# Optimization experiments

Hardware: AMD Instinct MI355X
Metric: run time of the kernel (lower is better)

The kernel has to match this reference:

```python
import jax, jax.numpy as jnp
import numpy as np

N_TASK, N_RET, N_DRAM, N_LINK = 50000, 20000, 5000, 100000
E_RET, E_DRAM, E_LINK = 1_000_000, 250_000, 2_000_000
H = 64


def setup_inputs() -> dict:
    key = jax.random.key(0)
    k = jax.random.split(key, 17)
    s = 1.0 / np.sqrt(3 * H)
    return {
        "feat_ret":  jax.random.normal(k[0], (E_RET, 1), jnp.float32),
        "feat_dram": jax.random.normal(k[1], (E_DRAM, 1), jnp.float32),
        "feat_link": jax.random.normal(k[2], (E_LINK, 1), jnp.float32),
        "W_ret":  jax.random.normal(k[3], (H, 1), jnp.float32),
        "b_ret":  jax.random.normal(k[4], (H,), jnp.float32) * 0.1,
        "W_dram": jax.random.normal(k[5], (H, 1), jnp.float32),
        "b_dram": jax.random.normal(k[6], (H,), jnp.float32) * 0.1,
        "W_link": jax.random.normal(k[7], (H, 1), jnp.float32),
        "b_link": jax.random.normal(k[8], (H,), jnp.float32) * 0.1,
        "W_task": jax.random.normal(k[9], (H, 3 * H), jnp.float32) * s,
        "b_task": jax.random.normal(k[10], (H,), jnp.float32) * 0.1,
        "task_ret":  jax.random.randint(k[11], (E_RET,), 0, N_TASK),
        "mod_ret":   jax.random.randint(k[12], (E_RET,), 0, N_RET),
        "task_dram": jax.random.randint(k[13], (E_DRAM,), 0, N_TASK),
        "mod_dram":  jax.random.randint(k[14], (E_DRAM,), 0, N_DRAM),
        "task_link": jax.random.randint(k[15], (E_LINK,), 0, N_TASK),
        "mod_link":  jax.random.randint(k[16], (E_LINK,), 0, N_LINK),
    }


def _gather_inp(feat, mod_idx, n_mod, W, b):
    # use_X: copy_e('feat') + sum per module node, then Linear(1,H) + tanh (activate_inp)
    inp = jax.ops.segment_sum(feat, mod_idx, num_segments=n_mod)  # [n_mod, 1]
    return jnp.tanh(inp @ W.T + b)                                # [n_mod, H]


def _max_to_task(inp_mod, mod_idx, task_idx, n_task):
    # X_used_by: copy_u('inp') + max per task node; zero-in-degree tasks -> 0 (DGL convention)
    m = jax.ops.segment_max(inp_mod[mod_idx], task_idx, num_segments=n_task)
    deg = jax.ops.segment_sum(jnp.ones_like(task_idx), task_idx, num_segments=n_task)
    return jnp.where((deg > 0)[:, None], m, 0.0)


def reference(feat_ret, feat_dram, feat_link, W_ret, b_ret, W_dram, b_dram,
              W_link, b_link, W_task, b_task,
              task_ret, mod_ret, task_dram, mod_dram, task_link, mod_link):
    # _module_update_inp
    inp_ret  = _gather_inp(feat_ret,  mod_ret,  N_RET,  W_ret,  b_ret)
    inp_dram = _gather_inp(feat_dram, mod_dram, N_DRAM, W_dram, b_dram)
    inp_link = _gather_inp(feat_link, mod_link, N_LINK, W_link, b_link)

    # _task_update_h: per-etype max reduce, cross-etype concat, Linear(3H,H) + tanh
    h_cat = jnp.concatenate([
        _max_to_task(inp_ret,  mod_ret,  task_ret,  N_TASK),
        _max_to_task(inp_dram, mod_dram, task_dram, N_TASK),
        _max_to_task(inp_link, mod_link, task_link, N_TASK),
    ], axis=-1)                                                   # [N_TASK, 3H]
    h_task = jnp.tanh(h_cat @ W_task.T + b_task)                  # [N_TASK, H]

    # _module_update_h: use_link copy_u('h') + mean per link node
    s = jax.ops.segment_sum(h_task[task_link], mod_link, num_segments=N_LINK)
    deg = jax.ops.segment_sum(jnp.ones((E_LINK,), jnp.float32), mod_link, num_segments=N_LINK)
    h_link = jnp.where((deg > 0)[:, None], s / jnp.maximum(deg, 1.0)[:, None], 0.0)
    return h_link
```

## Files before the change

kernel.cpp:

```cpp
#include <hip/hip_runtime.h>
#include <stdint.h>

#define N_TASK 50000
#define N_RET 20000
#define N_DRAM 5000
#define N_LINK 100000
#define E_RET 1000000
#define E_DRAM 250000
#define E_LINK 2000000

#define SBE 4096
#define NS_RET 245
#define NS_DRAM 62
#define NS_LINK 489
#define NS_TOT (NS_RET + NS_DRAM + NS_LINK)
#define MR_RET 64
#define RSZ_RET 313
#define MR_DRAM 16
#define RSZ_DRAM 313
#define MR_LINK 256
#define RSZ_LINK 391
#define RECIP313 107203u
#define RECIP391 85817u
#define CAPM_RET 16250
#define CAPM_DRAM 16250
#define CAPM_LINK 8255
#define BM4_RET 0
#define BM4_DRAM (MR_RET * NS_RET)
#define BM4_LINK (BM4_DRAM + MR_DRAM * NS_DRAM)
#define BM4_TOT (BM4_LINK + MR_LINK * NS_LINK)
#define BT_RET 0
#define BT_DRAM (16 * NS_RET)
#define BT_LINK (BT_DRAM + 16 * NS_DRAM)
#define BT_TOT (BT_LINK + 16 * NS_LINK)

#define R_PART 3125
#define CAP_RET 63800
#define CAP_DRAM 16300
#define CAP_LINK 126800
#define SUB_RET 4
#define SUB_DRAM 1
#define SUB_LINK 8
#define PB_RET 0
#define PB_DRAM (16 * SUB_RET * R_PART)
#define PB_LINK (PB_DRAM + 16 * SUB_DRAM * R_PART)
#define PB_TOT (PB_LINK + 16 * SUB_LINK * R_PART)

#define WS_SRET 0
#define WS_SDRAM 80000
#define WS_SLINK 100000
#define WS_CNT 500000
#define WS_OFFS 900000
#define WS_TMAX 1300000
#define WS_TMIN 1900000
#define WS_BCNT 2500000
#define WS_RCNT 2500192
#define WS_CSR 2501536
#define WS_BLKM 10501536
#define WS_BLKB 11068960
#define WS_MREC_RET 15701536
#define WS_MREC_DRAM 24021536
#define WS_MREC_LINK 26101536
#define WS_PART1 15701536
#define WS_HPL0_1 20901536
#define WS_HPL1_1 24101536
#define WS_TREC32_RET 43007776
#define WS_TREC32_DRAM 47090976
#define WS_TREC32_LINK 48134176
#define WS_WTB_1 56249376
#define WS_NEED1 56273952
#define WS_PART2 10501536
#define WS_TREC_RET 15701536
#define WS_TREC_DRAM 23867936
#define WS_TREC_LINK 25954336
#define WS_HPL0_2 15701536
#define WS_HPL1_2 18901536
#define WS_WTB_2 43007776
#define WS_NEED2 43032352

typedef __attribute__((ext_vector_type(8))) short bf16x8;
typedef __attribute__((ext_vector_type(4))) float f32x4;
typedef unsigned long long u64;

__device__ __forceinline__ unsigned ford(float f) {
  unsigned u = __float_as_uint(f);
  return (u & 0x80000000u) ? ~u : (u | 0x80000000u);
}
__device__ __forceinline__ float funord(unsigned t) {
  unsigned u = (t & 0x80000000u) ? (t & 0x7fffffffu) : ~t;
  return __uint_as_float(u);
}
__device__ __forceinline__ unsigned short bf16rne(float f) {
  unsigned u = __float_as_uint(f);
  return (unsigned short)((u + 0x7fffu + ((u >> 16) & 1u)) >> 16);
}

__device__ __forceinline__ void decode_sblk(int bx, int& e, int& blk, int& E0, int& NB,
                                            int& NR, unsigned& RECIP, int& RSZ, int& base) {
  if (bx < NS_RET) {
    e = 0; blk = bx; E0 = E_RET; NB = NS_RET; NR = MR_RET; RECIP = RECIP313; RSZ = RSZ_RET; base = BM4_RET;
  } else if (bx < NS_RET + NS_DRAM) {
    e = 1; blk = bx - NS_RET; E0 = E_DRAM; NB = NS_DRAM; NR = MR_DRAM; RECIP = RECIP313; RSZ = RSZ_DRAM; base = BM4_DRAM;
  } else {
    e = 2; blk = bx - NS_RET - NS_DRAM; E0 = E_LINK; NB = NS_LINK; NR = MR_LINK; RECIP = RECIP391; RSZ = RSZ_LINK; base = BM4_LINK;
  }
}
__device__ __forceinline__ void decode_stblk(int bx, int& e, int& blk, int& E0, int& NB,
                                             int& baset) {
  if (bx < NS_RET) { e = 0; blk = bx; E0 = E_RET; NB = NS_RET; baset = BT_RET; }
  else if (bx < NS_RET + NS_DRAM) { e = 1; blk = bx - NS_RET; E0 = E_DRAM; NB = NS_DRAM; baset = BT_DRAM; }
  else { e = 2; blk = bx - NS_RET - NS_DRAM; E0 = E_LINK; NB = NS_LINK; baset = BT_LINK; }
}


__global__ __launch_bounds__(256) void k_count3(
    const int* __restrict__ mr, const int* __restrict__ md, const int* __restrict__ ml,
    const float* __restrict__ W_task, unsigned short* __restrict__ wtb,
    int* __restrict__ blkcnt_m, int* __restrict__ tcur) {
  int bx = blockIdx.x, tid = threadIdx.x;
  if (bx == NS_TOT + 48) {
    if (tid < 48) tcur[tid] = 0;
    return;
  }
  if (bx >= NS_TOT) {
    int i = (bx - NS_TOT) * 256 + tid;
    if (i < 64 * 192) wtb[i] = bf16rne(W_task[i]);
    return;
  }
  __shared__ int c[256];
  int e, blk, E0, NB, NR, RSZ, base; unsigned RECIP;
  decode_sblk(bx, e, blk, E0, NB, NR, RECIP, RSZ, base);
  const int* mod = (e == 0) ? mr : (e == 1) ? md : ml;
  c[tid] = 0;
  __syncthreads();
  int i0 = blk * SBE;
#pragma unroll
  for (int q = 0; q < 16; q++) {
    int i = i0 + q * 256 + tid;
    if (i < E0) {
      int m = mod[i];
      int r = (int)(((u64)(unsigned)m * RECIP) >> 25);
      atomicAdd(&c[r], 1);
    }
  }
  __syncthreads();
  for (int r = tid; r < NR; r += 256)
    blkcnt_m[base + r * NB + blk] = c[r];
}

__global__ __launch_bounds__(512) void k_scan3(const int* __restrict__ blkcnt_m,
                                               int* __restrict__ blkbase_m,
                                               int* __restrict__ rcnt) {
  __shared__ int sm[512];
  int gb = blockIdx.x, tid = threadIdx.x;
  int NB, off;
  if (gb < 64) { NB = NS_RET; off = BM4_RET + gb * NS_RET; }
  else if (gb < 80) { NB = NS_DRAM; off = BM4_DRAM + (gb - 64) * NS_DRAM; }
  else { NB = NS_LINK; off = BM4_LINK + (gb - 80) * NS_LINK; }
  int v = (tid < NB) ? blkcnt_m[off + tid] : 0;
  sm[tid] = v;
  __syncthreads();
  for (int d = 1; d < 512; d <<= 1) {
    int x = (tid >= d) ? sm[tid - d] : 0;
    __syncthreads();
    sm[tid] += x;
    __syncthreads();
  }
  if (tid < NB) blkbase_m[off + tid] = sm[tid] - v;
  if (tid == 511) rcnt[gb] = sm[511];
}

__global__ __launch_bounds__(512) void k_mscatter3(
    const int* __restrict__ mr, const int* __restrict__ md, const int* __restrict__ ml,
    const int* __restrict__ tr, const int* __restrict__ td, const int* __restrict__ tl,
    const float* __restrict__ fr, const float* __restrict__ fd, const float* __restrict__ fl,
    const int* __restrict__ blkcnt_m, const int* __restrict__ blkbase_m,
    u64* __restrict__ mrec_ret, u64* __restrict__ mrec_dram, u64* __restrict__ mrec_link) {
  __shared__ int lcur[256];
  __shared__ int pdelta[256];
  __shared__ int sscan[256];
  __shared__ u64 srec[SBE];
  __shared__ int sdelta[SBE];
  int tid = threadIdx.x;
  int e, blk, E0, NB, NR, RSZ, base; unsigned RECIP;
  decode_sblk(blockIdx.x, e, blk, E0, NB, NR, RECIP, RSZ, base);
  const int* mod = (e == 0) ? mr : (e == 1) ? md : ml;
  const int* task = (e == 0) ? tr : (e == 1) ? td : tl;
  const float* feat = (e == 0) ? fr : (e == 1) ? fd : fl;
  u64* out = (e == 0) ? mrec_ret : (e == 1) ? mrec_dram : mrec_link;
  int CAP = (e == 0) ? CAPM_RET : (e == 1) ? CAPM_DRAM : CAPM_LINK;
  int cnt_r = 0, base_r = 0;
  if (tid < NR) {
    cnt_r = blkcnt_m[base + tid * NB + blk];
    base_r = blkbase_m[base + tid * NB + blk];
  }
  if (tid < 256) sscan[tid] = cnt_r;
  __syncthreads();
  for (int d = 1; d < 256; d <<= 1) {
    int x = (tid < 256 && tid >= d) ? sscan[tid - d] : 0;
    __syncthreads();
    if (tid < 256) sscan[tid] += x;
    __syncthreads();
  }
  if (tid < 256) {
    int excl = sscan[tid] - cnt_r;
    lcur[tid] = excl;
    pdelta[tid] = tid * CAP + base_r - excl;
  }
  __syncthreads();
  int i0 = blk * SBE;
#pragma unroll
  for (int q = 0; q < 8; q++) {
    int i = i0 + q * 512 + tid;
    if (i < E0) {
      int m = mod[i];
      int r = (int)(((u64)(unsigned)m * RECIP) >> 25);
      unsigned mloc = (unsigned)(m - r * RSZ);
      unsigned tk = (unsigned)task[i];
      unsigned fu = __float_as_uint(feat[i]);
      int slot = atomicAdd(&lcur[r], 1);
      srec[slot] = ((u64)fu << 32) | (tk << 16) | mloc;
      int gpos = pdelta[r] + slot - r * CAP;
      sdelta[slot] = (gpos < CAP) ? pdelta[r] : (int)0x80000000;
    }
  }
  __syncthreads();
  int total = E0 - i0; if (total > SBE) total = SBE;
  for (int s = tid; s < total; s += 512) {
    int d = sdelta[s];
    if (d != (int)0x80000000) out[d + s] = srec[s];
  }
}

#define P1BODY(rec, moff) { \
  int mloc_ = (int)((rec) & 0xFFFFull) + (moff); \
  int task_ = (int)(((rec) >> 16) & 0xFFFFull); \
  atomicAdd(&ssum[mloc_], __uint_as_float((unsigned)((rec) >> 32))); \
  if (e == 2) atomicAdd(&scnt[mloc_], 1); \
  atomicAdd(&tcnt16[w][task_ / R_PART], 1); }

#define P3BODY(rec, moff) { \
  int mloc_ = (int)((rec) & 0xFFFFull) + (moff); \
  int task_ = (int)(((rec) >> 16) & 0xFFFFull); \
  if (e == 2) { int lp_ = atomicAdd(&soff[mloc_], 1); csr[rb + lp_] = task_; } \
  int b_ = task_ / R_PART; \
  unsigned tl12_ = (unsigned)(task_ - b_ * R_PART); \
  unsigned u_ = (ford(ssum[mloc_]) & 0xFFFFF000u) | tl12_; \
  int local_ = atomicAdd(&tcnt16[w][b_], 1); \
  int pos_ = tbase16[w][b_] + local_; \
  if (pos_ < CAPT) trec[(long)b_ * CAPT + pos_] = u_; }

__global__ __launch_bounds__(1024) void k_msum3(
    const u64* __restrict__ mrec_ret, const u64* __restrict__ mrec_dram,
    const u64* __restrict__ mrec_link, const int* __restrict__ rcnt,
    int* __restrict__ cnt, int* __restrict__ offs, int* __restrict__ csr,
    int* __restrict__ tcur,
    unsigned* __restrict__ trec_ret, unsigned* __restrict__ trec_dram,
    unsigned* __restrict__ trec_link) {
  __shared__ float ssum[2 * RSZ_LINK];
  __shared__ int scnt[2 * RSZ_LINK];
  __shared__ int soff[2 * RSZ_LINK + 1];
  __shared__ int red[1024];
  __shared__ int tcnt16[16][16];
  __shared__ int tbase16[16][16];
  int gb = blockIdx.x, tid = threadIdx.x;
  int w = tid >> 6;
  int e, m0, nmod, RSZtot, CAPT, rl0 = 0;
  int cnt0, cnt1 = 0;
  const u64 *p0, *p1 = nullptr;
  unsigned* trec;
  if (gb < MR_RET) {
    e = 0; p0 = mrec_ret + (long)gb * CAPM_RET;
    cnt0 = rcnt[gb]; if (cnt0 > CAPM_RET) cnt0 = CAPM_RET;
    RSZtot = RSZ_RET; m0 = gb * RSZ_RET; nmod = N_RET - m0;
    CAPT = CAP_RET; trec = trec_ret;
  } else if (gb < MR_RET + MR_DRAM) {
    e = 1; int rl = gb - MR_RET; p0 = mrec_dram + (long)rl * CAPM_DRAM;
    cnt0 = rcnt[gb]; if (cnt0 > CAPM_DRAM) cnt0 = CAPM_DRAM;
    RSZtot = RSZ_DRAM; m0 = rl * RSZ_DRAM; nmod = N_DRAM - m0;
    CAPT = CAP_DRAM; trec = trec_dram;
  } else {
    e = 2; rl0 = 2 * (gb - (MR_RET + MR_DRAM));
    p0 = mrec_link + (long)rl0 * CAPM_LINK; p1 = p0 + CAPM_LINK;
    cnt0 = rcnt[80 + rl0]; if (cnt0 > CAPM_LINK) cnt0 = CAPM_LINK;
    cnt1 = rcnt[80 + rl0 + 1]; if (cnt1 > CAPM_LINK) cnt1 = CAPM_LINK;
    RSZtot = 2 * RSZ_LINK; m0 = rl0 * RSZ_LINK; nmod = N_LINK - m0;
    CAPT = CAP_LINK; trec = trec_link;
  }
  if (nmod > RSZtot) nmod = RSZtot;
  for (int j = tid; j < RSZtot; j += 1024) { ssum[j] = 0.f; scnt[j] = 0; }
  if (tid < 256) tcnt16[tid >> 4][tid & 15] = 0;
  __syncthreads();
  {
    int i = tid;
    for (; i + 3072 < cnt0; i += 4096) {
      u64 a = p0[i], b = p0[i + 1024], c = p0[i + 2048], d = p0[i + 3072];
      P1BODY(a, 0) P1BODY(b, 0) P1BODY(c, 0) P1BODY(d, 0)
    }
    for (; i < cnt0; i += 1024) { u64 a = p0[i]; P1BODY(a, 0) }
    if (e == 2) {
      i = tid;
      for (; i + 3072 < cnt1; i += 4096) {
        u64 a = p1[i], b = p1[i + 1024], c = p1[i + 2048], d = p1[i + 3072];
        P1BODY(a, RSZ_LINK) P1BODY(b, RSZ_LINK) P1BODY(c, RSZ_LINK) P1BODY(d, RSZ_LINK)
      }
      for (; i < cnt1; i += 1024) { u64 a = p1[i]; P1BODY(a, RSZ_LINK) }
    }
  }
  __syncthreads();
  if (tid < 16) {
    int b2 = tid, tot = 0;
    for (int w2 = 0; w2 < 16; w2++) { tbase16[w2][b2] = tot; tot += tcnt16[w2][b2]; }
    int g0 = atomicAdd(&tcur[e * 16 + b2], tot);
    for (int w2 = 0; w2 < 16; w2++) { tbase16[w2][b2] += g0; tcnt16[w2][b2] = 0; }
  }
  int rb = 0;
  if (e == 2) {
    int partial = (tid < 256 && tid < rl0) ? rcnt[80 + tid] : 0;
    if (tid < 256) red[tid] = partial;
    __syncthreads();
    for (int s = 128; s > 0; s >>= 1) {
      if (tid < s) red[tid] += red[tid + s];
      __syncthreads();
    }
    rb = red[0];
    __syncthreads();
    int vv = (tid < nmod) ? scnt[tid] : 0;
    red[tid] = vv;
    __syncthreads();
    for (int d = 1; d < 1024; d <<= 1) {
      int x = (tid >= d) ? red[tid - d] : 0;
      __syncthreads();
      red[tid] += x;
      __syncthreads();
    }
    if (tid < nmod) soff[tid] = red[tid] - vv;
    __syncthreads();
    for (int j = tid; j < nmod; j += 1024) {
      cnt[m0 + j] = scnt[j];
      offs[m0 + j] = rb + soff[j];
    }
  }
  __syncthreads();
  {
    int i = tid;
    for (; i + 3072 < cnt0; i += 4096) {
      u64 a = p0[i], b = p0[i + 1024], c = p0[i + 2048], d = p0[i + 3072];
      P3BODY(a, 0) P3BODY(b, 0) P3BODY(c, 0) P3BODY(d, 0)
    }
    for (; i < cnt0; i += 1024) { u64 a = p0[i]; P3BODY(a, 0) }
    if (e == 2) {
      i = tid;
      for (; i + 3072 < cnt1; i += 4096) {
        u64 a = p1[i], b = p1[i + 1024], c = p1[i + 2048], d = p1[i + 3072];
        P3BODY(a, RSZ_LINK) P3BODY(b, RSZ_LINK) P3BODY(c, RSZ_LINK) P3BODY(d, RSZ_LINK)
      }
      for (; i < cnt1; i += 1024) { u64 a = p1[i]; P3BODY(a, RSZ_LINK) }
    }
  }
}
#undef P1BODY
#undef P3BODY

#define PBBODY(rec) { \
  unsigned r_ = (rec) & 0xFFFu; \
  atomicMax(&lmax[r_], (rec)); \
  atomicMin(&lmin[r_], (rec)); }

__global__ __launch_bounds__(1024) void k_passb3(
    const unsigned* __restrict__ trec_ret, const unsigned* __restrict__ trec_dram,
    const unsigned* __restrict__ trec_link,
    const int* __restrict__ tcur, unsigned* __restrict__ partials) {
  __shared__ unsigned lmax[R_PART];
  __shared__ unsigned lmin[R_PART];
  int blk = blockIdx.x, tid = threadIdx.x;
  int e, b, sub, Nb, PB, CAP;
  const unsigned* bkt;
  if (blk < 16 * SUB_RET) {
    e = 0; b = blk >> 2; sub = blk & 3; Nb = SUB_RET; PB = PB_RET; CAP = CAP_RET; bkt = trec_ret;
  } else if (blk < 16 * (SUB_RET + SUB_DRAM)) {
    int q = blk - 16 * SUB_RET;
    e = 1; b = q; sub = 0; Nb = SUB_DRAM; PB = PB_DRAM; CAP = CAP_DRAM; bkt = trec_dram;
  } else {
    int q = blk - 16 * (SUB_RET + SUB_DRAM);
    e = 2; b = q >> 3; sub = q & 7; Nb = SUB_LINK; PB = PB_LINK; CAP = CAP_LINK; bkt = trec_link;
  }
  for (int idx = tid; idx < R_PART; idx += 1024) {
    lmax[idx] = 0u;
    lmin[idx] = 0xFFFFFFFFu;
  }
  __syncthreads();
  int count = tcur[e * 16 + b];
  if (count > CAP) count = CAP;
  int chunk = (count + Nb - 1) / Nb;
  int s0 = sub * chunk;
  int s1 = s0 + chunk; if (s1 > count) s1 = count;
  const unsigned* p = bkt + (long)b * CAP;
  int i = s0 + tid;
  for (; i + 3072 < s1; i += 4096) {
    unsigned r0 = p[i], r1 = p[i + 1024], r2 = p[i + 2048], r3 = p[i + 3072];
    PBBODY(r0) PBBODY(r1) PBBODY(r2) PBBODY(r3)
  }
  for (; i < s1; i += 1024) { unsigned r0 = p[i]; PBBODY(r0) }
  __syncthreads();
  unsigned gbase = PB + (unsigned)(b * Nb + sub) * R_PART;
  for (int idx = tid; idx < R_PART; idx += 1024) {
    partials[gbase + idx] = lmax[idx];
    partials[PB_TOT + gbase + idx] = lmin[idx];
  }
}
#undef PBBODY

__global__ __launch_bounds__(256) void k_mmred3(const unsigned* __restrict__ partials,
                                                unsigned* __restrict__ tmax,
                                                unsigned* __restrict__ tmin) {
  int gid = blockIdx.x * 256 + threadIdx.x;
  if (gid >= 3 * N_TASK) return;
  int e = gid / N_TASK;
  int t = gid - e * N_TASK;
  int Nb = (e == 0) ? SUB_RET : (e == 1) ? SUB_DRAM : SUB_LINK;
  int PB = (e == 0) ? PB_RET : (e == 1) ? PB_DRAM : PB_LINK;
  int b = t / R_PART;
  int r = t - b * R_PART;
  unsigned umax = 0u, umin = 0xFFFFFFFFu;
  for (int sub = 0; sub < Nb; sub++) {
    unsigned idx = PB + (unsigned)(b * Nb + sub) * R_PART + r;
    unsigned wv = partials[idx];
    if (wv > umax) umax = wv;
    unsigned w2 = partials[PB_TOT + idx];
    if (w2 < umin) umin = w2;
  }
  tmax[gid] = umax & 0xFFFFF000u;
  tmin[gid] = umin & 0xFFFFF000u;
}


__global__ __launch_bounds__(256) void k_count(
    const int* __restrict__ mr, const int* __restrict__ md, const int* __restrict__ ml,
    const int* __restrict__ tr, const int* __restrict__ td, const int* __restrict__ tl,
    const float* __restrict__ W_task, unsigned short* __restrict__ wtb,
    int* __restrict__ blkcnt_m, int* __restrict__ blkcnt_t) {
  int bx = blockIdx.x, tid = threadIdx.x;
  if (bx >= 2 * NS_TOT) {
    int i = (bx - 2 * NS_TOT) * 256 + tid;
    if (i < 64 * 192) wtb[i] = bf16rne(W_task[i]);
    return;
  }
  __shared__ int c[256];
  c[tid] = 0;
  __syncthreads();
  if (bx < NS_TOT) {
    int e, blk, E0, NB, NR, RSZ, base; unsigned RECIP;
    decode_sblk(bx, e, blk, E0, NB, NR, RECIP, RSZ, base);
    const int* mod = (e == 0) ? mr : (e == 1) ? md : ml;
    int i0 = blk * SBE;
#pragma unroll
    for (int q = 0; q < 16; q++) {
      int i = i0 + q * 256 + tid;
      if (i < E0) {
        int m = mod[i];
        int r = (int)(((u64)(unsigned)m * RECIP) >> 25);
        atomicAdd(&c[r], 1);
      }
    }
    __syncthreads();
    for (int r = tid; r < NR; r += 256)
      blkcnt_m[base + r * NB + blk] = c[r];
  } else {
    int e, blk, E0, NB, baset;
    decode_stblk(bx - NS_TOT, e, blk, E0, NB, baset);
    const int* task = (e == 0) ? tr : (e == 1) ? td : tl;
    int i0 = blk * SBE;
#pragma unroll
    for (int q = 0; q < 16; q++) {
      int i = i0 + q * 256 + tid;
      if (i < E0) atomicAdd(&c[task[i] / R_PART], 1);
    }
    __syncthreads();
    if (tid < 16) blkcnt_t[baset + tid * NB + blk] = c[tid];
  }
}

__global__ __launch_bounds__(512) void k_scan(int* __restrict__ blkcnt_m,
                                              int* __restrict__ blkcnt_t,
                                              int* __restrict__ rcnt, int* __restrict__ bcnt) {
  __shared__ int sm[512];
  int gb = blockIdx.x, tid = threadIdx.x;
  int* arr; int NB; int* outp;
  if (gb < 336) {
    int off;
    if (gb < 64) { NB = NS_RET; off = BM4_RET + gb * NS_RET; }
    else if (gb < 80) { NB = NS_DRAM; off = BM4_DRAM + (gb - 64) * NS_DRAM; }
    else { NB = NS_LINK; off = BM4_LINK + (gb - 80) * NS_LINK; }
    arr = blkcnt_m + off; outp = rcnt + gb;
  } else {
    int g = gb - 336; int e = g >> 4, b = g & 15;
    int NBe = (e == 0) ? NS_RET : (e == 1) ? NS_DRAM : NS_LINK;
    int baset = (e == 0) ? BT_RET : (e == 1) ? BT_DRAM : BT_LINK;
    NB = NBe; arr = blkcnt_t + baset + b * NBe; outp = bcnt + g;
  }
  int v = (tid < NB) ? arr[tid] : 0;
  sm[tid] = v;
  __syncthreads();
  for (int d = 1; d < 512; d <<= 1) {
    int x = (tid >= d) ? sm[tid - d] : 0;
    __syncthreads();
    sm[tid] += x;
    __syncthreads();
  }
  if (tid < NB) arr[tid] = sm[tid] - v;
  if (tid == 511) *outp = sm[511];
}

__global__ __launch_bounds__(256) void k_mscatter2(
    const int* __restrict__ mr, const int* __restrict__ md, const int* __restrict__ ml,
    const int* __restrict__ tl,
    const float* __restrict__ fr, const float* __restrict__ fd, const float* __restrict__ fl,
    const int* __restrict__ blkcnt_m,
    u64* __restrict__ mrec_ret, u64* __restrict__ mrec_dram, u64* __restrict__ mrec_link) {
  __shared__ int lcur[256];
  __shared__ int pdelta[256];
  __shared__ int sscan[256];
  __shared__ u64 srec[SBE];
  __shared__ int sdelta[SBE];
  int tid = threadIdx.x;
  int e, blk, E0, NB, NR, RSZ, base; unsigned RECIP;
  decode_sblk(blockIdx.x, e, blk, E0, NB, NR, RECIP, RSZ, base);
  const int* mod = (e == 0) ? mr : (e == 1) ? md : ml;
  const float* feat = (e == 0) ? fr : (e == 1) ? fd : fl;
  u64* out = (e == 0) ? mrec_ret : (e == 1) ? mrec_dram : mrec_link;
  int CAP = (e == 0) ? CAPM_RET : (e == 1) ? CAPM_DRAM : CAPM_LINK;
  lcur[tid] = 0;
  __syncthreads();
  int i0 = blk * SBE;
#pragma unroll
  for (int q = 0; q < 16; q++) {
    int i = i0 + q * 256 + tid;
    if (i < E0) {
      int m = mod[i];
      int r = (int)(((u64)(unsigned)m * RECIP) >> 25);
      atomicAdd(&lcur[r], 1);
    }
  }
  __syncthreads();
  int v = lcur[tid];
  sscan[tid] = v;
  __syncthreads();
  for (int d = 1; d < 256; d <<= 1) {
    int x = (tid >= d) ? sscan[tid - d] : 0;
    __syncthreads();
    sscan[tid] += x;
    __syncthreads();
  }
  int excl = sscan[tid] - v;
  int total = sscan[255];
  int gbv = (tid < NR) ? blkcnt_m[base + tid * NB + blk] : 0;
  __syncthreads();
  lcur[tid] = excl;
  pdelta[tid] = tid * CAP + gbv - excl;
  __syncthreads();
#pragma unroll
  for (int q = 0; q < 16; q++) {
    int i = i0 + q * 256 + tid;
    if (i < E0) {
      int m = mod[i];
      int r = (int)(((u64)(unsigned)m * RECIP) >> 25);
      unsigned mloc = (unsigned)(m - r * RSZ);
      unsigned task = (e == 2) ? (unsigned)tl[i] : 0u;
      unsigned fu = __float_as_uint(feat[i]);
      int slot = atomicAdd(&lcur[r], 1);
      srec[slot] = ((u64)fu << 32) | (task << 16) | mloc;
      int gpos = pdelta[r] + slot - r * CAP;
      sdelta[slot] = (gpos < CAP) ? pdelta[r] : (int)0x80000000;
    }
  }
  __syncthreads();
  for (int s = tid; s < total; s += 256) {
    int d = sdelta[s];
    if (d != (int)0x80000000) out[d + s] = srec[s];
  }
}

__global__ __launch_bounds__(256) void k_msum(
    const u64* __restrict__ mrec_ret, const u64* __restrict__ mrec_dram,
    const u64* __restrict__ mrec_link, const int* __restrict__ rcnt,
    float* __restrict__ s_ret, float* __restrict__ s_dram, float* __restrict__ s_link,
    int* __restrict__ cnt, int* __restrict__ offs, int* __restrict__ csr) {
  __shared__ float ssum[RSZ_LINK];
  __shared__ int scnt[RSZ_LINK];
  __shared__ int soff[RSZ_LINK + 1];
  __shared__ int red[256];
  int gb = blockIdx.x, tid = threadIdx.x;
  int e, rl, RSZ, CAP, Ntot;
  const u64* p;
  float* sout;
  if (gb < MR_RET) {
    e = 0; rl = gb; p = mrec_ret + (long)rl * CAPM_RET; sout = s_ret;
    RSZ = RSZ_RET; CAP = CAPM_RET; Ntot = N_RET;
  } else if (gb < MR_RET + MR_DRAM) {
    e = 1; rl = gb - MR_RET; p = mrec_dram + (long)rl * CAPM_DRAM; sout = s_dram;
    RSZ = RSZ_DRAM; CAP = CAPM_DRAM; Ntot = N_DRAM;
  } else {
    e = 2; rl = gb - MR_RET - MR_DRAM; p = mrec_link + (long)rl * CAPM_LINK; sout = s_link;
    RSZ = RSZ_LINK; CAP = CAPM_LINK; Ntot = N_LINK;
  }
  int m0 = rl * RSZ;
  int nmod = Ntot - m0; if (nmod > RSZ) nmod = RSZ;
  for (int j = tid; j < RSZ; j += 256) { ssum[j] = 0.f; scnt[j] = 0; }
  __syncthreads();
  int count = rcnt[gb]; if (count > CAP) count = CAP;
  for (int i = tid; i < count; i += 256) {
    u64 rec = p[i];
    int mloc = (int)(rec & 0xFFFFull);
    atomicAdd(&ssum[mloc], __uint_as_float((unsigned)(rec >> 32)));
    if (e == 2) atomicAdd(&scnt[mloc], 1);
  }
  __syncthreads();
  for (int j = tid; j < nmod; j += 256) sout[m0 + j] = ssum[j];
  if (e != 2) return;
  int partial = (80 + tid < gb) ? rcnt[80 + tid] : 0;
  red[tid] = partial;
  __syncthreads();
  for (int s = 128; s > 0; s >>= 1) {
    if (tid < s) red[tid] += red[tid + s];
    __syncthreads();
  }
  int rb = red[0];
  __syncthreads();
  int a0 = (2 * tid < nmod) ? scnt[2 * tid] : 0;
  int a1 = (2 * tid + 1 < nmod) ? scnt[2 * tid + 1] : 0;
  red[tid] = a0 + a1;
  __syncthreads();
  for (int d = 1; d < 256; d <<= 1) {
    int x = (tid >= d) ? red[tid - d] : 0;
    __syncthreads();
    red[tid] += x;
    __syncthreads();
  }
  int excl = red[tid] - (a0 + a1);
  if (2 * tid < RSZ_LINK) soff[2 * tid] = excl;
  if (2 * tid + 1 < RSZ_LINK) soff[2 * tid + 1] = excl + a0;
  __syncthreads();
  for (int j = tid; j < nmod; j += 256) {
    cnt[m0 + j] = scnt[j];
    offs[m0 + j] = rb + soff[j];
  }
  __syncthreads();
  for (int i = tid; i < count; i += 256) {
    u64 rec = p[i];
    int mloc = (int)(rec & 0xFFFFull);
    int task = (int)((rec >> 16) & 0xFFFFull);
    int lp = atomicAdd(&soff[mloc], 1);
    csr[rb + lp] = task;
  }
}

__global__ __launch_bounds__(256) void k_ascatter2(
    const int* __restrict__ tr, const int* __restrict__ mr,
    const int* __restrict__ td, const int* __restrict__ md,
    const int* __restrict__ tl, const int* __restrict__ ml,
    const float* __restrict__ s_ret, const float* __restrict__ s_dram,
    const float* __restrict__ s_link, const int* __restrict__ blkcnt_t,
    u64* __restrict__ trec_ret, u64* __restrict__ trec_dram, u64* __restrict__ trec_link) {
  __shared__ int lcur[256];
  __shared__ int pdelta[256];
  __shared__ int sscan[256];
  __shared__ u64 srec[SBE];
  __shared__ int sdelta[SBE];
  int tid = threadIdx.x;
  int e, blk, E0, NB, baset;
  decode_stblk(blockIdx.x, e, blk, E0, NB, baset);
  const int* task = (e == 0) ? tr : (e == 1) ? td : tl;
  const int* mod = (e == 0) ? mr : (e == 1) ? md : ml;
  const float* s = (e == 0) ? s_ret : (e == 1) ? s_dram : s_link;
  u64* out = (e == 0) ? trec_ret : (e == 1) ? trec_dram : trec_link;
  int CAP = (e == 0) ? CAP_RET : (e == 1) ? CAP_DRAM : CAP_LINK;
  lcur[tid] = 0;
  __syncthreads();
  int i0 = blk * SBE;
#pragma unroll
  for (int q = 0; q < 16; q++) {
    int i = i0 + q * 256 + tid;
    if (i < E0) atomicAdd(&lcur[task[i] / R_PART], 1);
  }
  __syncthreads();
  int v = lcur[tid];
  sscan[tid] = v;
  __syncthreads();
  for (int d = 1; d < 256; d <<= 1) {
    int x = (tid >= d) ? sscan[tid - d] : 0;
    __syncthreads();
    sscan[tid] += x;
    __syncthreads();
  }
  int excl = sscan[tid] - v;
  int total = sscan[255];
  int gbv = (tid < 16) ? blkcnt_t[baset + tid * NB + blk] : 0;
  __syncthreads();
  lcur[tid] = excl;
  pdelta[tid] = tid * CAP + gbv - excl;
  __syncthreads();
#pragma unroll
  for (int q = 0; q < 16; q++) {
    int i = i0 + q * 256 + tid;
    if (i < E0) {
      int t = task[i];
      int r = t / R_PART;
      unsigned rloc = (unsigned)(t - r * R_PART);
      unsigned u = ford(s[mod[i]]);
      int slot = atomicAdd(&lcur[r], 1);
      srec[slot] = ((u64)u << 32) | rloc;
      int gpos = pdelta[r] + slot - r * CAP;
      sdelta[slot] = (gpos < CAP) ? pdelta[r] : (int)0x80000000;
    }
  }
  __syncthreads();
  for (int sidx = tid; sidx < total; sidx += 256) {
    int d = sdelta[sidx];
    if (d != (int)0x80000000) out[d + sidx] = srec[sidx];
  }
}

__global__ __launch_bounds__(256) void k_passb(
    const u64* __restrict__ trec_ret, const u64* __restrict__ trec_dram,
    const u64* __restrict__ trec_link,
    const int* __restrict__ bcnt, unsigned* __restrict__ partials) {
  __shared__ unsigned lmax[R_PART];
  __shared__ unsigned lmin[R_PART];
  int blk = blockIdx.x;
  int e, b, sub, Nb, PB, CAP;
  const u64* bkt;
  if (blk < 16 * SUB_RET) {
    e = 0; b = blk >> 2; sub = blk & 3; Nb = SUB_RET; PB = PB_RET; CAP = CAP_RET; bkt = trec_ret;
  } else if (blk < 16 * (SUB_RET + SUB_DRAM)) {
    int q = blk - 16 * SUB_RET;
    e = 1; b = q; sub = 0; Nb = SUB_DRAM; PB = PB_DRAM; CAP = CAP_DRAM; bkt = trec_dram;
  } else {
    int q = blk - 16 * (SUB_RET + SUB_DRAM);
    e = 2; b = q >> 3; sub = q & 7; Nb = SUB_LINK; PB = PB_LINK; CAP = CAP_LINK; bkt = trec_link;
  }
  for (int idx = threadIdx.x; idx < R_PART; idx += 256) {
    lmax[idx] = 0u;
    lmin[idx] = 0xFFFFFFFFu;
  }
  __syncthreads();
  int count = bcnt[e * 16 + b];
  if (count > CAP) count = CAP;
  int chunk = (count + Nb - 1) / Nb;
  int s0 = sub * chunk;
  int s1 = s0 + chunk; if (s1 > count) s1 = count;
  const u64* p = bkt + (long)b * CAP;
  for (int i = s0 + threadIdx.x; i < s1; i += 256) {
    u64 rec = p[i];
    unsigned r = (unsigned)rec;
    unsigned u = (unsigned)(rec >> 32);
    atomicMax(&lmax[r], u);
    atomicMin(&lmin[r], u);
  }
  __syncthreads();
  unsigned gbase = PB + (unsigned)(b * Nb + sub) * R_PART;
  for (int idx = threadIdx.x; idx < R_PART; idx += 256) {
    partials[gbase + idx] = lmax[idx];
    partials[PB_TOT + gbase + idx] = lmin[idx];
  }
}

__global__ __launch_bounds__(256) void k_mmred2(const unsigned* __restrict__ partials,
                                                unsigned* __restrict__ tmax,
                                                unsigned* __restrict__ tmin) {
  int gid = blockIdx.x * 256 + threadIdx.x;
  if (gid >= 3 * N_TASK) return;
  int e = gid / N_TASK;
  int t = gid - e * N_TASK;
  int Nb = (e == 0) ? SUB_RET : (e == 1) ? SUB_DRAM : SUB_LINK;
  int PB = (e == 0) ? PB_RET : (e == 1) ? PB_DRAM : PB_LINK;
  int b = t / R_PART;
  int r = t - b * R_PART;
  unsigned umax = 0u, umin = 0xFFFFFFFFu;
  for (int sub = 0; sub < Nb; sub++) {
    unsigned idx = PB + (unsigned)(b * Nb + sub) * R_PART + r;
    unsigned wv = partials[idx];
    if (wv > umax) umax = wv;
    unsigned w2 = partials[PB_TOT + idx];
    if (w2 < umin) umin = w2;
  }
  tmax[gid] = umax;
  tmin[gid] = umin;
}


__global__ void k_wprep(const float* __restrict__ W_task, unsigned short* __restrict__ wtb) {
  int i = blockIdx.x * 256 + threadIdx.x;
  if (i < 64 * 192) wtb[i] = bf16rne(W_task[i]);
}

__global__ void f_segsum(const float* __restrict__ fr, const float* __restrict__ fd,
                         const float* __restrict__ fl,
                         const int* __restrict__ mr, const int* __restrict__ md,
                         const int* __restrict__ ml,
                         float* s_ret, float* s_dram, float* s_link, int* cnt) {
  int i = blockIdx.x * blockDim.x + threadIdx.x;
  const int total = E_RET + E_DRAM + E_LINK;
  if (i >= total) return;
  if (i < E_RET) {
    atomicAdd(&s_ret[mr[i]], fr[i]);
  } else if (i < E_RET + E_DRAM) {
    int j = i - E_RET;
    atomicAdd(&s_dram[md[j]], fd[j]);
  } else {
    int j = i - (E_RET + E_DRAM);
    int m = ml[j];
    atomicAdd(&s_link[m], fl[j]);
    atomicAdd(&cnt[m], 1);
  }
}

__global__ void f_minmax(const float* __restrict__ s_ret, const float* __restrict__ s_dram,
                         const float* __restrict__ s_link,
                         const int* __restrict__ tr, const int* __restrict__ mr,
                         const int* __restrict__ td, const int* __restrict__ md,
                         const int* __restrict__ tl, const int* __restrict__ ml,
                         unsigned* tmax, unsigned* tmin) {
  int i = blockIdx.x * blockDim.x + threadIdx.x;
  const int total = E_RET + E_DRAM + E_LINK;
  if (i >= total) return;
  int e, task; unsigned u;
  if (i < E_RET) {
    u = ford(s_ret[mr[i]]); task = tr[i]; e = 0;
  } else if (i < E_RET + E_DRAM) {
    int j = i - E_RET;
    u = ford(s_dram[md[j]]); task = td[j]; e = 1;
  } else {
    int j = i - (E_RET + E_DRAM);
    u = ford(s_link[ml[j]]); task = tl[j]; e = 2;
  }
  atomicMax(&tmax[e * N_TASK + task], u);
  atomicMin(&tmin[e * N_TASK + task], u);
}

__global__ void f_part(const int* __restrict__ cnt, int* part) {
  __shared__ int sm[256];
  int i = blockIdx.x * 256 + threadIdx.x;
  sm[threadIdx.x] = (i < N_LINK) ? cnt[i] : 0;
  __syncthreads();
  for (int s = 128; s > 0; s >>= 1) {
    if (threadIdx.x < s) sm[threadIdx.x] += sm[threadIdx.x + s];
    __syncthreads();
  }
  if (threadIdx.x == 0) part[blockIdx.x] = sm[0];
}

__global__ void f_scanpart(const int* __restrict__ part, int* partx, int npart) {
  __shared__ int sm[512];
  int t = threadIdx.x;
  int v = (t < npart) ? part[t] : 0;
  sm[t] = v;
  __syncthreads();
  for (int d = 1; d < 512; d <<= 1) {
    int x = (t >= d) ? sm[t - d] : 0;
    __syncthreads();
    sm[t] += x;
    __syncthreads();
  }
  if (t < npart) partx[t] = sm[t] - v;
}

__global__ void f_offs(const int* __restrict__ cnt, const int* __restrict__ partx,
                       int* offs, int* cursor) {
  __shared__ int sm[256];
  int i = blockIdx.x * 256 + threadIdx.x;
  int t = threadIdx.x;
  int v = (i < N_LINK) ? cnt[i] : 0;
  sm[t] = v;
  __syncthreads();
  for (int d = 1; d < 256; d <<= 1) {
    int x = (t >= d) ? sm[t - d] : 0;
    __syncthreads();
    sm[t] += x;
    __syncthreads();
  }
  if (i < N_LINK) {
    int o = partx[blockIdx.x] + sm[t] - v;
    offs[i] = o;
    cursor[i] = o;
  }
}

__global__ void f_scatter(const int* __restrict__ tl, const int* __restrict__ ml,
                          int* cursor, int* csr) {
  int i = blockIdx.x * blockDim.x + threadIdx.x;
  if (i >= E_LINK) return;
  int pos = atomicAdd(&cursor[ml[i]], 1);
  csr[pos] = tl[i];
}


__global__ __launch_bounds__(256) void k_taskm(
    const float* __restrict__ W_ret, const float* __restrict__ b_ret,
    const float* __restrict__ W_dram, const float* __restrict__ b_dram,
    const float* __restrict__ W_link, const float* __restrict__ b_link,
    const unsigned short* __restrict__ wtb, const float* __restrict__ b_task,
    const unsigned* __restrict__ tmax, const unsigned* __restrict__ tmin,
    unsigned short* __restrict__ hp0, unsigned short* __restrict__ hp1) {
  int wave = threadIdx.x >> 6;
  int lane = threadIdx.x & 63;
  int tile = blockIdx.x * 4 + wave;
  if (tile >= N_TASK / 16) return;
  int t0 = tile * 16;
  int l16 = lane & 15;
  int quad = lane >> 4;
  int t = t0 + l16;

  f32x4 acc[4];
#pragma unroll
  for (int nf = 0; nf < 4; nf++) acc[nf] = (f32x4){0.f, 0.f, 0.f, 0.f};

  const float* We[3] = {W_ret, W_dram, W_link};
  const float* be[3] = {b_ret, b_dram, b_link};

  for (int e = 0; e < 3; e++) {
    unsigned um = tmax[e * N_TASK + t];
    float smax = funord(um);
    float smin = funord(tmin[e * N_TASK + t]);
    bool live = (um != 0u);
#pragma unroll
    for (int h = 0; h < 2; h++) {
      int kb = h * 32 + quad * 8;
      float4 w0 = *(const float4*)&We[e][kb];
      float4 w1 = *(const float4*)&We[e][kb + 4];
      float4 b0 = *(const float4*)&be[e][kb];
      float4 b1 = *(const float4*)&be[e][kb + 4];
      float wv[8] = {w0.x, w0.y, w0.z, w0.w, w1.x, w1.y, w1.z, w1.w};
      float bv[8] = {b0.x, b0.y, b0.z, b0.w, b1.x, b1.y, b1.z, b1.w};
      bf16x8 afrag;
#pragma unroll
      for (int j = 0; j < 8; j++) {
        float wj = wv[j];
        float ss = (wj >= 0.f) ? smax : smin;
        float hc = live ? tanhf(fmaf(ss, wj, bv[j])) : 0.f;
        afrag[j] = (short)bf16rne(hc);
      }
      int kk = e * 64 + h * 32 + quad * 8;
#pragma unroll
      for (int nf = 0; nf < 4; nf++) {
        int o = nf * 16 + l16;
        bf16x8 bfrag = *(const bf16x8*)&wtb[o * 192 + kk];
        acc[nf] = __builtin_amdgcn_mfma_f32_16x16x32_bf16(afrag, bfrag, acc[nf], 0, 0, 0);
      }
    }
  }

#pragma unroll
  for (int nf = 0; nf < 4; nf++) {
    int n = nf * 16 + l16;
    float bt = b_task[n];
    unsigned short* hp = (n < 32) ? hp0 : hp1;
    int f = n & 31;
#pragma unroll
    for (int r = 0; r < 4; r++) {
      int m = quad * 4 + r;
      float v = tanhf(acc[nf][r] + bt);
      hp[(t0 + m) * 32 + f] = bf16rne(v);
    }
  }
}

__global__ __launch_bounds__(256) void k_link2(const unsigned short* __restrict__ hp,
                                               const int* __restrict__ offs,
                                               const int* __restrict__ cnt,
                                               const int* __restrict__ csr,
                                               float* __restrict__ out, int plane) {
  int l = blockIdx.x * 8 + (threadIdx.x >> 5);
  int f = threadIdx.x & 31;
  int start = offs[l];
  int c = cnt[l];
  float acc = 0.f;
  for (int q = 0; q < c; q += 4) {
    int i1 = (q + 1 < c) ? q + 1 : c - 1;
    int i2 = (q + 2 < c) ? q + 2 : c - 1;
    int i3 = (q + 3 < c) ? q + 3 : c - 1;
    int t0 = csr[start + q];
    int t1 = csr[start + i1];
    int t2 = csr[start + i2];
    int t3 = csr[start + i3];
    unsigned v0 = hp[t0 * 32 + f];
    unsigned v1 = hp[t1 * 32 + f];
    unsigned v2 = hp[t2 * 32 + f];
    unsigned v3 = hp[t3 * 32 + f];
    acc += __uint_as_float(v0 << 16);
    if (q + 1 < c) acc += __uint_as_float(v1 << 16);
    if (q + 2 < c) acc += __uint_as_float(v2 << 16);
    if (q + 3 < c) acc += __uint_as_float(v3 << 16);
  }
  out[l * 64 + plane * 32 + f] = (c > 0) ? acc / (float)c : 0.f;
}

extern "C" void kernel_launch(void* const* d_in, const int* in_sizes, int n_in,
                              void* d_out, int out_size, void* d_ws, size_t ws_size,
                              hipStream_t stream) {
  const float* feat_ret  = (const float*)d_in[0];
  const float* feat_dram = (const float*)d_in[1];
  const float* feat_link = (const float*)d_in[2];
  const float* W_ret  = (const float*)d_in[3];
  const float* b_ret  = (const float*)d_in[4];
  const float* W_dram = (const float*)d_in[5];
  const float* b_dram = (const float*)d_in[6];
  const float* W_link = (const float*)d_in[7];
  const float* b_link = (const float*)d_in[8];
  const float* W_task = (const float*)d_in[9];
  const float* b_task = (const float*)d_in[10];
  const int* task_ret  = (const int*)d_in[11];
  const int* mod_ret   = (const int*)d_in[12];
  const int* task_dram = (const int*)d_in[13];
  const int* mod_dram  = (const int*)d_in[14];
  const int* task_link = (const int*)d_in[15];
  const int* mod_link  = (const int*)d_in[16];
  float* out = (float*)d_out;

  char* ws = (char*)d_ws;
  float* s_ret  = (float*)(ws + WS_SRET);
  float* s_dram = (float*)(ws + WS_SDRAM);
  float* s_link = (float*)(ws + WS_SLINK);
  int*   cnt    = (int*)(ws + WS_CNT);
  int*   offs   = (int*)(ws + WS_OFFS);
  unsigned* tmax = (unsigned*)(ws + WS_TMAX);
  unsigned* tmin = (unsigned*)(ws + WS_TMIN);
  int* tcur = (int*)(ws + WS_BCNT);
  int* rcnt = (int*)(ws + WS_RCNT);
  int* csr  = (int*)(ws + WS_CSR);
  int* blkcnt_m = (int*)(ws + WS_BLKM);
  int* blkb = (int*)(ws + WS_BLKB);
  u64* mrec_ret  = (u64*)(ws + WS_MREC_RET);
  u64* mrec_dram = (u64*)(ws + WS_MREC_DRAM);
  u64* mrec_link = (u64*)(ws + WS_MREC_LINK);

  unsigned short* hp0;
  unsigned short* hp1;
  unsigned short* wtb;

  if (ws_size >= (size_t)WS_NEED1) {
    unsigned* partials = (unsigned*)(ws + WS_PART1);
    unsigned* trec_ret  = (unsigned*)(ws + WS_TREC32_RET);
    unsigned* trec_dram = (unsigned*)(ws + WS_TREC32_DRAM);
    unsigned* trec_link = (unsigned*)(ws + WS_TREC32_LINK);
    hp0 = (unsigned short*)(ws + WS_HPL0_1);
    hp1 = (unsigned short*)(ws + WS_HPL1_1);
    wtb = (unsigned short*)(ws + WS_WTB_1);
    k_count3<<<NS_TOT + 49, 256, 0, stream>>>(mod_ret, mod_dram, mod_link,
                                              W_task, wtb, blkcnt_m, tcur);
    k_scan3<<<336, 512, 0, stream>>>(blkcnt_m, blkb, rcnt);
    k_mscatter3<<<NS_TOT, 512, 0, stream>>>(mod_ret, mod_dram, mod_link,
                                            task_ret, task_dram, task_link,
                                            feat_ret, feat_dram, feat_link,
                                            blkcnt_m, blkb,
                                            mrec_ret, mrec_dram, mrec_link);
    k_msum3<<<MR_RET + MR_DRAM + MR_LINK / 2, 1024, 0, stream>>>(
        mrec_ret, mrec_dram, mrec_link, rcnt,
        cnt, offs, csr, tcur,
        trec_ret, trec_dram, trec_link);
    k_passb3<<<16 * (SUB_RET + SUB_DRAM + SUB_LINK), 1024, 0, stream>>>(
        trec_ret, trec_dram, trec_link, tcur, partials);
    k_mmred3<<<(3 * N_TASK + 255) / 256, 256, 0, stream>>>(partials, tmax, tmin);
  } else if (ws_size >= (size_t)WS_NEED2) {
    unsigned* partials = (unsigned*)(ws + WS_PART2);
    u64* trec_ret  = (u64*)(ws + WS_TREC_RET);
    u64* trec_dram = (u64*)(ws + WS_TREC_DRAM);
    u64* trec_link = (u64*)(ws + WS_TREC_LINK);
    hp0 = (unsigned short*)(ws + WS_HPL0_2);
    hp1 = (unsigned short*)(ws + WS_HPL1_2);
    wtb = (unsigned short*)(ws + WS_WTB_2);
    k_count<<<2 * NS_TOT + 48, 256, 0, stream>>>(mod_ret, mod_dram, mod_link,
                                                 task_ret, task_dram, task_link,
                                                 W_task, wtb, blkcnt_m, blkb);
    k_scan<<<384, 512, 0, stream>>>(blkcnt_m, blkb, rcnt, tcur);
    k_mscatter2<<<NS_TOT, 256, 0, stream>>>(mod_ret, mod_dram, mod_link, task_link,
                                            feat_ret, feat_dram, feat_link, blkcnt_m,
                                            mrec_ret, mrec_dram, mrec_link);
    k_msum<<<336, 256, 0, stream>>>(mrec_ret, mrec_dram, mrec_link, rcnt,
                                    s_ret, s_dram, s_link, cnt, offs, csr);
    k_ascatter2<<<NS_TOT, 256, 0, stream>>>(task_ret, mod_ret, task_dram, mod_dram,
                                            task_link, mod_link, s_ret, s_dram, s_link,
                                            blkb, trec_ret, trec_dram, trec_link);
    k_passb<<<16 * (SUB_RET + SUB_DRAM + SUB_LINK), 256, 0, stream>>>(
        trec_ret, trec_dram, trec_link, tcur, partials);
    k_mmred2<<<(3 * N_TASK + 255) / 256, 256, 0, stream>>>(partials, tmax, tmin);
  } else {
    int* part   = (int*)(ws + WS_BLKM);
    int* partx  = (int*)(ws + WS_BLKM + 4096);
    int* cursor = (int*)(ws + WS_BLKB);
    hp0 = (unsigned short*)(ws + WS_HPL0_2);
    hp1 = (unsigned short*)(ws + WS_HPL1_2);
    wtb = (unsigned short*)(ws + WS_WTB_2);
    hipMemsetAsync(ws, 0, 1900000, stream);
    hipMemsetAsync(ws + WS_TMIN, 0xFF, 600000, stream);
    const int totalE = E_RET + E_DRAM + E_LINK;
    int nblk_e = (totalE + 255) / 256;
    f_segsum<<<nblk_e, 256, 0, stream>>>(feat_ret, feat_dram, feat_link,
                                         mod_ret, mod_dram, mod_link,
                                         s_ret, s_dram, s_link, cnt);
    f_minmax<<<nblk_e, 256, 0, stream>>>(s_ret, s_dram, s_link,
                                         task_ret, mod_ret, task_dram, mod_dram,
                                         task_link, mod_link, tmax, tmin);
    const int npart = (N_LINK + 255) / 256;
    f_part<<<npart, 256, 0, stream>>>(cnt, part);
    f_scanpart<<<1, 512, 0, stream>>>(part, partx, npart);
    f_offs<<<npart, 256, 0, stream>>>(cnt, partx, offs, cursor);
    f_scatter<<<(E_LINK + 255) / 256, 256, 0, stream>>>(task_link, mod_link, cursor, csr);
    k_wprep<<<48, 256, 0, stream>>>(W_task, wtb);
  }

  k_taskm<<<(N_TASK / 16 + 3) / 4, 256, 0, stream>>>(W_ret, b_ret, W_dram, b_dram,
                                                     W_link, b_link, wtb, b_task,
                                                     tmax, tmin, hp0, hp1);
  k_link2<<<N_LINK / 8, 256, 0, stream>>>(hp0, offs, cnt, csr, out, 0);
  k_link2<<<N_LINK / 8, 256, 0, stream>>>(hp1, offs, cnt, csr, out, 1);
}
```

Before: 293.7 us.

## Stage per-bucket task records and CSR in LDS, store CSR as 16-bit

k_msum3 now writes task records and link CSR entries into shared-memory staging buffers, then copies them out to global memory contiguously per bucket. This replaces scattered per-record global stores with coalesced ones. The CSR task index array also becomes unsigned short, which halves its storage and the read traffic in k_link2. The cost is a large LDS footprint (about 99KB), which may limit occupancy or exceed the LDS limit, and staging relies on per-block counts fitting within MS_STAGE.

```diff
diff --git a/kernel.cpp b/kernel.cpp
--- a/kernel.cpp
+++ b/kernel.cpp
@@ -78,6 +78,8 @@
 #define WS_WTB_2 43007776
 #define WS_NEED2 43032352
 
+#define MS_STAGE 16512
+
 typedef __attribute__((ext_vector_type(8))) short bf16x8;
 typedef __attribute__((ext_vector_type(4))) float f32x4;
 typedef unsigned long long u64;
@@ -242,18 +244,17 @@
 #define P3BODY(rec, moff) { \
   int mloc_ = (int)((rec) & 0xFFFFull) + (moff); \
   int task_ = (int)(((rec) >> 16) & 0xFFFFull); \
-  if (e == 2) { int lp_ = atomicAdd(&soff[mloc_], 1); csr[rb + lp_] = task_; } \
+  if (e == 2) { int lp_ = atomicAdd(&soff[mloc_], 1); scsr2[lp_] = (unsigned short)task_; } \
   int b_ = task_ / R_PART; \
   unsigned tl12_ = (unsigned)(task_ - b_ * R_PART); \
   unsigned u_ = (ford(ssum[mloc_]) & 0xFFFFF000u) | tl12_; \
   int local_ = atomicAdd(&tcnt16[w][b_], 1); \
-  int pos_ = tbase16[w][b_] + local_; \
-  if (pos_ < CAPT) trec[(long)b_ * CAPT + pos_] = u_; }
+  strec[lbase[b_] + tbase16[w][b_] + local_] = u_; }
 
 __global__ __launch_bounds__(1024) void k_msum3(
     const u64* __restrict__ mrec_ret, const u64* __restrict__ mrec_dram,
     const u64* __restrict__ mrec_link, const int* __restrict__ rcnt,
-    int* __restrict__ cnt, int* __restrict__ offs, int* __restrict__ csr,
+    int* __restrict__ cnt, int* __restrict__ offs, unsigned short* __restrict__ csr,
     int* __restrict__ tcur,
     unsigned* __restrict__ trec_ret, unsigned* __restrict__ trec_dram,
     unsigned* __restrict__ trec_link) {
@@ -263,6 +264,9 @@
   __shared__ int red[1024];
   __shared__ int tcnt16[16][16];
   __shared__ int tbase16[16][16];
+  __shared__ int g0s[16], tot16[16], lbase[16];
+  __shared__ unsigned strec[MS_STAGE];
+  __shared__ unsigned short scsr2[MS_STAGE];
   int gb = blockIdx.x, tid = threadIdx.x;
   int w = tid >> 6;
   int e, m0, nmod, RSZtot, CAPT, rl0 = 0;
@@ -311,8 +315,14 @@
   if (tid < 16) {
     int b2 = tid, tot = 0;
     for (int w2 = 0; w2 < 16; w2++) { tbase16[w2][b2] = tot; tot += tcnt16[w2][b2]; }
-    int g0 = atomicAdd(&tcur[e * 16 + b2], tot);
-    for (int w2 = 0; w2 < 16; w2++) { tbase16[w2][b2] += g0; tcnt16[w2][b2] = 0; }
+    tot16[b2] = tot;
+    g0s[b2] = atomicAdd(&tcur[e * 16 + b2], tot);
+    for (int w2 = 0; w2 < 16; w2++) tcnt16[w2][b2] = 0;
+  }
+  __syncthreads();
+  if (tid == 0) {
+    int run = 0;
+    for (int b2 = 0; b2 < 16; b2++) { lbase[b2] = run; run += tot16[b2]; }
   }
   int rb = 0;
   if (e == 2) {
@@ -357,6 +367,20 @@
       }
       for (; i < cnt1; i += 1024) { u64 a = p1[i]; P3BODY(a, RSZ_LINK) }
     }
+  }
+  __syncthreads();
+  for (int b = 0; b < 16; b++) {
+    int g0b = g0s[b];
+    int kmax = tot16[b];
+    int rem = CAPT - g0b; if (rem < 0) rem = 0;
+    if (kmax > rem) kmax = rem;
+    unsigned* dst = trec + (long)b * CAPT + g0b;
+    const unsigned* src = strec + lbase[b];
+    for (int k = tid; k < kmax; k += 1024) dst[k] = src[k];
+  }
+  if (e == 2) {
+    int ctot = cnt0 + cnt1;
+    for (int k = tid; k < ctot; k += 1024) csr[rb + k] = scsr2[k];
   }
 }
 #undef P1BODY
@@ -585,7 +609,7 @@
     const u64* __restrict__ mrec_ret, const u64* __restrict__ mrec_dram,
     const u64* __restrict__ mrec_link, const int* __restrict__ rcnt,
     float* __restrict__ s_ret, float* __restrict__ s_dram, float* __restrict__ s_link,
-    int* __restrict__ cnt, int* __restrict__ offs, int* __restrict__ csr) {
+    int* __restrict__ cnt, int* __restrict__ offs, unsigned short* __restrict__ csr) {
   __shared__ float ssum[RSZ_LINK];
   __shared__ int scnt[RSZ_LINK];
   __shared__ int soff[RSZ_LINK + 1];
@@ -651,7 +675,7 @@
     int mloc = (int)(rec & 0xFFFFull);
     int task = (int)((rec >> 16) & 0xFFFFull);
     int lp = atomicAdd(&soff[mloc], 1);
-    csr[rb + lp] = task;
+    csr[rb + lp] = (unsigned short)task;
   }
 }
 
@@ -887,11 +911,11 @@
 }
 
 __global__ void f_scatter(const int* __restrict__ tl, const int* __restrict__ ml,
-                          int* cursor, int* csr) {
+                          int* cursor, unsigned short* csr) {
   int i = blockIdx.x * blockDim.x + threadIdx.x;
   if (i >= E_LINK) return;
   int pos = atomicAdd(&cursor[ml[i]], 1);
-  csr[pos] = tl[i];
+  csr[pos] = (unsigned short)tl[i];
 }
 
 
@@ -968,7 +992,7 @@
 __global__ __launch_bounds__(256) void k_link2(const unsigned short* __restrict__ hp,
                                                const int* __restrict__ offs,
                                                const int* __restrict__ cnt,
-                                               const int* __restrict__ csr,
+                                               const unsigned short* __restrict__ csr,
                                                float* __restrict__ out, int plane) {
   int l = blockIdx.x * 8 + (threadIdx.x >> 5);
   int f = threadIdx.x & 31;
@@ -1027,7 +1051,7 @@
   unsigned* tmin = (unsigned*)(ws + WS_TMIN);
   int* tcur = (int*)(ws + WS_BCNT);
   int* rcnt = (int*)(ws + WS_RCNT);
-  int* csr  = (int*)(ws + WS_CSR);
+  unsigned short* csr = (unsigned short*)(ws + WS_CSR);
   int* blkcnt_m = (int*)(ws + WS_BLKM);
   int* blkb = (int*)(ws + WS_BLKB);
   u64* mrec_ret  = (u64*)(ws + WS_MREC_RET);
```

New measurement: 282.6 us. -3.8%, faster.
